# Kernel tuning notes

Measured on AMD Instinct MI355X. Metric: run time of the kernel, lower is better.

The kernel has to match this reference:

```python
import jax, jax.numpy as jnp
import numpy as np

B, S, D, I, C = 4, 512, 512, 1024, 64
BASE_LR = 0.01
EPS = 1e-6


def _rms(x, w):
    return x * jax.lax.rsqrt(jnp.mean(x * x, axis=-1, keepdims=True) + EPS) * w


def _mem_apply(p, x):
    # 2-layer MLP memory: x + RMSNorm(W1 @ silu(W0 @ x))
    h = jax.nn.silu(x @ p["w0"].T)
    y = h @ p["w1"].T
    return x + _rms(y, p["ln"])


def _mem_loss(p, inp, tgt, w):
    # ((target - pred)^2 * theta).mean(-1).sum() over batch; w is scalar theta_t
    pred = _mem_apply(p, inp)
    return jnp.sum(jnp.mean((tgt - pred) ** 2 * w, axis=-1))


def _neural_memory(x, wq, wk, wv, q_norm_w, k_norm_w, alpha_w, alpha_b,
                   theta_w, theta_b, eta_w, eta_b, m_w0, m_w1, m_ln):
    b, s, d = x.shape
    nC = s // C
    params0 = {"w0": m_w0, "w1": m_w1, "ln": m_ln}
    surpr0 = jax.tree_util.tree_map(jnp.zeros_like, params0)
    xs = x.reshape(b, nC, C, d).transpose(1, 0, 2, 3)  # [nC, B, C, D]

    # per-token grads: vmap over sequence dim 1, shared params (in_dims=None)
    grad_fn = jax.vmap(jax.grad(_mem_loss), in_axes=(None, 1, 1, 0))
    idx = jnp.arange(C)

    def step(carry, xc):
        params, surpr = carry
        # adaptive gates: Linear -> sum over batch -> sigmoid (shapes [C])
        al = jax.nn.sigmoid(jnp.sum(xc @ alpha_w.T + alpha_b, axis=0))[:, 0]
        th = jax.nn.sigmoid(jnp.sum(xc @ theta_w.T + theta_b, axis=0))[:, 0] * BASE_LR
        et = jax.nn.sigmoid(jnp.sum(xc @ eta_w.T + eta_b, axis=0))[:, 0]
        k = _rms(jax.nn.silu(xc @ wk.T), k_norm_w)  # [B, C, D]
        v = jax.nn.silu(xc @ wv.T)
        grads = grad_fn(params, k, v, th)  # each leaf [C, *param_shape]
        # eta decay matrix E[m,n] = prod_{i=n+1}^m eta_i for n<=m, else 0
        M0 = jnp.where(idx[:, None] > idx[None, :], et[:, None], 1.0)
        Emat = jnp.where(idx[None, :] <= idx[:, None], jnp.cumprod(M0, axis=0), 0.0)
        c_eta = jnp.cumprod(et)  # prod_{0..m} eta
        beta = 1.0 - al
        bc_last = jnp.cumprod(beta)[-1]
        bt = jnp.cumprod(beta[::-1])[::-1]  # bt[m] = prod_{m..C-1} beta
        w_beta = jnp.concatenate([bt[1:], jnp.ones((1,), et.dtype)])

        def upd(pS, pM, u):
            # S_t = eta_t * S_{t-1} - u_t ; M_t = beta_t * M_{t-1} + S_t (vectorized)
            ex = (slice(None),) + (None,) * pS.ndim
            S_all = c_eta[ex] * pS - jnp.einsum("mn,n...->m...", Emat, u)
            newM = pM * bc_last + jnp.einsum("m,m...->...", w_beta, S_all)
            return newM, S_all[-1]

        res = {n: upd(surpr[n], params[n], grads[n]) for n in params}
        new_params = {n: res[n][0] for n in params}
        new_surpr = {n: res[n][1] for n in params}
        return (new_params, new_surpr), None

    (paramsF, _surprF), _ = jax.lax.scan(step, (params0, surpr0), xs)
    # retrieve from updated memory
    q = _rms(jax.nn.silu(x @ wq.T), q_norm_w)
    return _mem_apply(paramsF, q)


def setup_inputs() -> dict:
    key = jax.random.key(0)
    ks = jax.random.split(key, 12)

    def xavier(k, shape):
        lim = float(np.sqrt(6.0 / (shape[0] + shape[1])))
        return jax.random.uniform(k, shape, jnp.float32, -lim, lim)

    return {
        "x": jax.random.normal(ks[0], (B, S, D), jnp.float32),
        "wq": xavier(ks[1], (D, D)),
        "wk": xavier(ks[2], (D, D)),
        "wv": xavier(ks[3], (D, D)),
        "q_norm_w": jnp.ones((D,), jnp.float32),
        "k_norm_w": jnp.ones((D,), jnp.float32),
        "alpha_w": xavier(ks[4], (1, D)),
        "alpha_b": jnp.zeros((1,), jnp.float32),
        "theta_w": xavier(ks[5], (1, D)),
        "theta_b": jnp.zeros((1,), jnp.float32),
        "eta_w": xavier(ks[6], (1, D)),
        "eta_b": jnp.zeros((1,), jnp.float32),
        "m_w0": xavier(ks[7], (I, D)),
        "m_w1": xavier(ks[8], (D, I)),
        "m_ln": jnp.ones((D,), jnp.float32),
    }


def reference(x, wq, wk, wv, q_norm_w, k_norm_w, alpha_w, alpha_b,
              theta_w, theta_b, eta_w, eta_b, m_w0, m_w1, m_ln):
    return _neural_memory(x, wq, wk, wv, q_norm_w, k_norm_w, alpha_w, alpha_b,
                          theta_w, theta_b, eta_w, eta_b, m_w0, m_w1, m_ln)
```

## Files before the change

### kernel.cpp

```cpp
#include <hip/hip_runtime.h>
#include <math.h>

#define EPS 1e-6f

namespace {

typedef unsigned short u16;
typedef unsigned int u32;
typedef __bf16 bf16x8 __attribute__((ext_vector_type(8)));
typedef float f32x4 __attribute__((ext_vector_type(4)));
typedef u16 u16x8 __attribute__((ext_vector_type(8)));

constexpr int Bb = 4, Ss = 512, Dd = 512, Ii = 1024, Cc = 64;
constexpr int nCk = 8, RowsC = 256, RowsAll = 2048;

__device__ __forceinline__ float sigmoidf_(float x) { return 1.f / (1.f + expf(-x)); }
__device__ __forceinline__ float siluf_(float x)    { return x / (1.f + expf(-x)); }

__device__ __forceinline__ u16 f2bf(float f) {
  u32 u = __float_as_uint(f);
  u32 r = u + 0x7fffu + ((u >> 16) & 1u);
  return (u16)(r >> 16);
}

__device__ __forceinline__ void llds16(const u16* g, u16* l) {
  __builtin_amdgcn_global_load_lds((__attribute__((address_space(1))) void*)g,
                                   (__attribute__((address_space(3))) void*)l,
                                   16, 0, 0);
}

__device__ __forceinline__ void drain_barrier() {
  asm volatile("s_waitcnt vmcnt(0)" ::: "memory");
  __builtin_amdgcn_s_barrier();
}

__device__ __forceinline__ float wave_sum(float v) {
  #pragma unroll
// ... 2 lines not shown
}

__device__ __forceinline__ float block_reduce_sum(float v, float* red) {
  int tid = threadIdx.x;
  red[tid] = v; __syncthreads();
  for (int s = 128; s > 0; s >>= 1) {
    if (tid < s) red[tid] += red[tid + s];
    __syncthreads();
  }
  float r = red[0]; __syncthreads();
  return r;
}

struct WS {
  float *w0c, *Sw0, *w1c, *Sw1, *lnc, *Sln, *tmpK, *Krows, *Vrows,
        *Ybuf, *gyr, *Z0, *alv, *thv, *etv, *wBv, *wEv, *scal, *Qb, *Yr;
  u16 *xcb, *wqb, *wkvb, *w0b, *w1b, *w1tb, *Kb, *KT, *Hb, *Ht,
      *dYb, *dYtW, *dYtE, *dHtW, *dHtE, *Qbb, *Hrb;
};
__host__ __device__ inline WS mkws(char* base) {
  WS s; char* p = base + 256;
#define CF(nm, n) s.nm = (float*)p; p += (size_t)(n) * 4;
#define CU(nm, n) s.nm = (u16*)p;   p += (size_t)(n) * 2;
  CF(w0c, Ii*Dd) CF(Sw0, Ii*Dd) CF(w1c, Dd*Ii) CF(Sw1, Dd*Ii)
  CF(lnc, Dd) CF(Sln, Dd)
  CF(tmpK, (size_t)RowsAll*Dd) CF(Krows, (size_t)RowsAll*Dd) CF(Vrows, (size_t)RowsAll*Dd)
  CF(Ybuf, RowsC*Dd) CF(gyr, RowsC*Dd) CF(Z0, RowsC*Ii)
  CF(alv, Ss) CF(thv, Ss) CF(etv, Ss) CF(wBv, nCk*RowsC) CF(wEv, nCk*RowsC) CF(scal, nCk*4)
  CF(Qb, (size_t)RowsAll*Dd) CF(Yr, (size_t)RowsAll*Dd)
  CU(xcb, (size_t)RowsAll*Dd) CU(wqb, Dd*Dd) CU(wkvb, (size_t)Ii*Dd)
  CU(w0b, (size_t)Ii*Dd) CU(w1b, (size_t)Dd*Ii) CU(w1tb, (size_t)Ii*Dd)
  CU(Kb, (size_t)RowsAll*Dd) CU(KT, (size_t)RowsAll*Dd)
  CU(Hb, RowsC*Ii) CU(Ht, RowsC*Ii)
  CU(dYb, RowsC*Dd) CU(dYtW, RowsC*Dd) CU(dYtE, RowsC*Dd)
  CU(dHtW, RowsC*Ii) CU(dHtE, RowsC*Ii)
  CU(Qbb, (size_t)RowsAll*Dd) CU(Hrb, (size_t)RowsAll*Ii)
#undef CF
#undef CU
  return s;
}

template<int BK, int EPI>
__device__ void tile64(
    u16* smA, u16* smB,
    const u16* __restrict__ A, const u16* __restrict__ Bt,
    int K, int N, int bm, int bn,
    float* C0, float* C1, u16* Cb, u16* CbT, u16* CbT2,
    const float* Z, const float* wB, const float* wE, int trM)
{
  constexpr int CPR = BK / 8;
  constexpr int NISS = (64 * CPR) / 256;
  constexpr int BUF = 64 * BK;
  const int tid = threadIdx.x;
  const int l = tid & 63, lr = l & 15, lq = l >> 4;
  const int w = tid >> 6, wr = w >> 1, wc = w & 1;

  f32x4 acc[2][2];
  #pragma unroll
  for (int i = 0; i < 2; ++i)
    #pragma unroll
    for (int j = 0; j < 2; ++j) acc[i][j] = f32x4{0.f, 0.f, 0.f, 0.f};

  auto stage = [&](int k0, int buf) {
// ... 1 lines not shown
    u16* dB = smB + buf * BUF;
    #pragma unroll
    for (int i = 0; i < NISS; ++i) {
      int e = i * 256 + tid;
      int r = e / CPR, c = (e & (CPR - 1)) ^ (r & (CPR - 1));
      llds16(A  + (size_t)(bm + r) * K + k0 + c * 8, dA + e * 8);
      llds16(Bt + (size_t)(bn + r) * K + k0 + c * 8, dB + e * 8);
    }
  };

  stage(0, 0);
  drain_barrier();
  const int nt = K / BK;
  int cur = 0;
  for (int t = 0; t < nt; ++t) {
    if (t + 1 < nt) stage((t + 1) * BK, cur ^ 1);
    const u16* sA = smA + cur * BUF;
    const u16* sB = smB + cur * BUF;
    #pragma unroll
    for (int kk = 0; kk < BK / 32; ++kk) {
      bf16x8 av[2], bv[2];
      #pragma unroll
      for (int m = 0; m < 2; ++m) {
        int r = wr * 32 + m * 16 + lr;
        int c = (kk * 4 + lq) ^ (r & (CPR - 1));
        av[m] = *reinterpret_cast<const bf16x8*>(&sA[r * BK + c * 8]);
      }
      #pragma unroll
      for (int n = 0; n < 2; ++n) {
        int r = wc * 32 + n * 16 + lr;
        int c = (kk * 4 + lq) ^ (r & (CPR - 1));
        bv[n] = *reinterpret_cast<const bf16x8*>(&sB[r * BK + c * 8]);
      }
      #pragma unroll
      for (int m = 0; m < 2; ++m)
        #pragma unroll
        for (int n = 0; n < 2; ++n)
          acc[m][n] = __builtin_amdgcn_mfma_f32_16x16x32_bf16(av[m], bv[n], acc[m][n], 0, 0, 0);
    }
    drain_barrier();
    cur ^= 1;
  }

  #pragma unroll
  for (int m = 0; m < 2; ++m) {
    int gr0 = bm + wr * 32 + m * 16 + lq * 4;
    float wbq[4], weq[4];
    if (EPI == 3) {
      #pragma unroll
      for (int q = 0; q < 4; ++q) { wbq[q] = wB[gr0 + q]; weq[q] = wE[gr0 + q]; }
    }
    #pragma unroll
    for (int n = 0; n < 2; ++n) {
      int gc = bn + wc * 32 + n * 16 + lr;
      ushort4 t1, t2;
      #pragma unroll
      for (int q = 0; q < 4; ++q) {
        float v = acc[m][n][q];
        size_t idx = (size_t)(gr0 + q) * N + gc;
        if (EPI == 0) {
          C0[idx] = v;
        } else if (EPI == 1) {
          if (gc < Dd) C0[(size_t)(gr0 + q) * Dd + gc] = v;
          else         C1[(size_t)(gr0 + q) * Dd + gc - Dd] = siluf_(v);
        } else if (EPI == 2) {
          C0[idx] = v;
          float h = siluf_(v);
          Cb[idx] = f2bf(h);
          ((u16*)&t1)[q] = f2bf(h);
        } else if (EPI == 3) {
          float z = Z[idx];
          float sg = 1.f / (1.f + expf(-z));
          float dh = v * sg * (1.f + z * (1.f - sg));
          ((u16*)&t1)[q] = f2bf(dh * wbq[q]);
          ((u16*)&t2)[q] = f2bf(dh * weq[q]);
        } else if (EPI == 4) {
          Cb[idx] = f2bf(siluf_(v));
        }
      }
      if (EPI == 2) *reinterpret_cast<ushort4*>(&CbT[(size_t)gc * trM + gr0]) = t1;
      if (EPI == 3) {
        *reinterpret_cast<ushort4*>(&CbT[(size_t)gc * trM + gr0]) = t1;
        *reinterpret_cast<ushort4*>(&CbT2[(size_t)gc * trM + gr0]) = t2;
      }
    }
  }
}

template<int BK, bool TR>
__device__ void gtile64(
    u16* smA, u16* smB, u16* smE,
    const u16* __restrict__ AW, const u16* __restrict__ AE,
    const u16* __restrict__ Bt,
    float* P, float* Sm, u16* Pb, u16* PbT, const float* scal,
    int M, int N, int K, int bm, int bn)
{
  constexpr int CPR = BK / 8;
  constexpr int NISS = (64 * CPR) / 256;
  constexpr int BUF = 64 * BK;
  const int tid = threadIdx.x;
  const int l = tid & 63, lr = l & 15, lq = l >> 4;
  const int w = tid >> 6, wr = w >> 1, wc = w & 1;

  f32x4 aM[2][2], aE[2][2];
// ... 12 lines not shown
    #pragma unroll
    for (int i = 0; i < NISS; ++i) {
      int e = i * 256 + tid;
      int r = e / CPR, c = (e & (CPR - 1)) ^ (r & (CPR - 1));
      llds16(AW + (size_t)(bm + r) * K + k0 + c * 8, dA + e * 8);
      llds16(AE + (size_t)(bm + r) * K + k0 + c * 8, dE + e * 8);
      llds16(Bt + (size_t)(bn + r) * K + k0 + c * 8, dB + e * 8);
    }
  };

  stage(0, 0);
  drain_barrier();
  const int nt = K / BK;
  int cur = 0;
  for (int t = 0; t < nt; ++t) {
    if (t + 1 < nt) stage((t + 1) * BK, cur ^ 1);
    const u16* sA = smA + cur * BUF;
    const u16* sE = smE + cur * BUF;
    const u16* sB = smB + cur * BUF;
    #pragma unroll
    for (int kk = 0; kk < BK / 32; ++kk) {
      bf16x8 awv[2], aev[2], bv[2];
      #pragma unroll
      for (int m = 0; m < 2; ++m) {
        int r = wr * 32 + m * 16 + lr;
        int c = (kk * 4 + lq) ^ (r & (CPR - 1));
        awv[m] = *reinterpret_cast<const bf16x8*>(&sA[r * BK + c * 8]);
        aev[m] = *reinterpret_cast<const bf16x8*>(&sE[r * BK + c * 8]);
      }
      #pragma unroll
      for (int n = 0; n < 2; ++n) {
        int r = wc * 32 + n * 16 + lr;
        int c = (kk * 4 + lq) ^ (r & (CPR - 1));
        bv[n] = *reinterpret_cast<const bf16x8*>(&sB[r * BK + c * 8]);
      }
      #pragma unroll
      for (int m = 0; m < 2; ++m)
        #pragma unroll
        for (int n = 0; n < 2; ++n) {
          aM[m][n] = __builtin_amdgcn_mfma_f32_16x16x32_bf16(awv[m], bv[n], aM[m][n], 0, 0, 0);
          aE[m][n] = __builtin_amdgcn_mfma_f32_16x16x32_bf16(aev[m], bv[n], aE[m][n], 0, 0, 0);
        }
    }
    drain_barrier();
    cur ^= 1;
  }

  float s0 = scal[0], s1 = scal[1], s2 = scal[2];
  #pragma unroll
  for (int m = 0; m < 2; ++m) {
    int gr0 = bm + wr * 32 + m * 16 + lq * 4;
    #pragma unroll
    for (int n = 0; n < 2; ++n) {
      int gc = bn + wc * 32 + n * 16 + lr;
      ushort4 t1;
      #pragma unroll
      for (int q = 0; q < 4; ++q) {
        size_t idx = (size_t)(gr0 + q) * N + gc;
        float p = P[idx], s = Sm[idx];
        float np = s0 * p + s1 * s - aM[m][n][q];
        float ns = s2 * s - aE[m][n][q];
        P[idx] = np; Sm[idx] = ns;
        Pb[idx] = f2bf(np);
        if (TR) ((u16*)&t1)[q] = f2bf(np);
      }
      if (TR) *reinterpret_cast<ushort4*>(&PbT[(size_t)gc * M + gr0]) = t1;
    }
  }
}

template<int BK, int EPI>
__global__ __launch_bounds__(256) void mgemm_k(
    const u16* __restrict__ A, const u16* __restrict__ Bt,
    float* C0, float* C1, u16* Cb, u16* CbT, u16* CbT2,
    const float* Z, const float* wB, const float* wE,
    int M, int N, int K, int trM)
{
  __shared__ __align__(16) u16 sm[4 * 64 * BK];
  tile64<BK, EPI>(sm, sm + 2 * 64 * BK, A, Bt, K, N,
                  blockIdx.y * 64, blockIdx.x * 64,
                  C0, C1, Cb, CbT, CbT2, Z, wB, wE, trM);
}

template<int EPI>
__global__ __launch_bounds__(256) void mgemm128_k(
    const u16* __restrict__ A, const u16* __restrict__ Bt,
    float* C0, u16* Cb, int M, int N, int K)
{
  constexpr int TS = 128, BK = 64;
  constexpr int BUF = TS * BK;
  __shared__ __align__(16) u16 As[2 * BUF];
  __shared__ __align__(16) u16 Bs[2 * BUF];
  const int tid = threadIdx.x;
  const int l = tid & 63, lr = l & 15, lq = l >> 4;
  const int w = tid >> 6, wr = w >> 1, wc = w & 1;
  const int bm = blockIdx.y * TS, bn = blockIdx.x * TS;

  f32x4 acc[4][4];
  #pragma unroll
  for (int i = 0; i < 4; ++i)
    #pragma unroll
    for (int j = 0; j < 4; ++j) acc[i][j] = f32x4{0.f, 0.f, 0.f, 0.f};

  auto stage = [&](int k0, int buf) {
    u16* dA = As + buf * BUF;
    u16* dB = Bs + buf * BUF;
    #pragma unroll
    for (int i = 0; i < 4; ++i) {
      int e = i * 256 + tid;
      int r = e >> 3, c = (e & 7) ^ (r & 7);
      llds16(A  + (size_t)(bm + r) * K + k0 + c * 8, dA + e * 8);
      llds16(Bt + (size_t)(bn + r) * K + k0 + c * 8, dB + e * 8);
    }
  };

  stage(0, 0);
  drain_barrier();
  const int nt = K / BK;
  int cur = 0;
  for (int t = 0; t < nt; ++t) {
    if (t + 1 < nt) stage((t + 1) * BK, cur ^ 1);
    const u16* sA = As + cur * BUF;
    const u16* sB = Bs + cur * BUF;
    #pragma unroll
    for (int kk = 0; kk < 2; ++kk) {
      bf16x8 av[4], bv[4];
      #pragma unroll
      for (int m = 0; m < 4; ++m) {
        int r = wr * 64 + m * 16 + lr;
        int c = (kk * 4 + lq) ^ (r & 7);
        av[m] = *reinterpret_cast<const bf16x8*>(&sA[r * BK + c * 8]);
      }
      #pragma unroll
      for (int n = 0; n < 4; ++n) {
        int r = wc * 64 + n * 16 + lr;
        int c = (kk * 4 + lq) ^ (r & 7);
        bv[n] = *reinterpret_cast<const bf16x8*>(&sB[r * BK + c * 8]);
      }
      #pragma unroll
      for (int m = 0; m < 4; ++m)
        #pragma unroll
        for (int n = 0; n < 4; ++n)
          acc[m][n] = __builtin_amdgcn_mfma_f32_16x16x32_bf16(av[m], bv[n], acc[m][n], 0, 0, 0);
    }
    drain_barrier();
    cur ^= 1;
  }

  #pragma unroll
  for (int m = 0; m < 4; ++m) {
    int gr0 = bm + wr * 64 + m * 16 + lq * 4;
    #pragma unroll
    for (int n = 0; n < 4; ++n) {
      int gc = bn + wc * 64 + n * 16 + lr;
      #pragma unroll
      for (int q = 0; q < 4; ++q) {
        size_t idx = (size_t)(gr0 + q) * N + gc;
        float v = acc[m][n][q];
        if (EPI == 0) C0[idx] = v;
        else          Cb[idx] = f2bf(siluf_(v));
      }
    }
  }
}

template<int BK>
__global__ __launch_bounds__(256) void dh_colsum_k(
    const u16* __restrict__ dYb, const u16* __restrict__ w1tb,
    u16* dHtW, u16* dHtE, const float* Z0,
    const float* wB, const float* wE,
    const float* gyr, float* lnc, float* Sln, const float* scal)
{
  __shared__ __align__(16) u16 sm[4 * 64 * BK];
  int j = blockIdx.x;
  if (j < 64) {
    int tm = j & 3, tn = j >> 2;
    tile64<BK, 3>(sm, sm + 2 * 64 * BK, dYb, w1tb, Dd, Ii, tm * 64, tn * 64,
                  nullptr, nullptr, nullptr, dHtW, dHtE, Z0, wB, wE, RowsC);
  } else {
    int d = (j - 64) * 256 + threadIdx.x;
    float sm2 = 0.f, se2 = 0.f;
    for (int r = 0; r < RowsC; ++r) {
      float vv = gyr[(size_t)r * Dd + d];
      sm2 += wB[r] * vv; se2 += wE[r] * vv;
    }
    float pp = lnc[d], sn = Sln[d];
    lnc[d] = scal[0] * pp + scal[1] * sn - sm2;
    Sln[d] = scal[2] * sn - se2;
  }
}

template<int BK>
__global__ __launch_bounds__(256) void g2_k(
    const u16* __restrict__ dYtW, const u16* __restrict__ dYtE,
    const u16* __restrict__ Ht,
    const u16* __restrict__ dHtW, const u16* __restrict__ dHtE,
    const u16* __restrict__ KTc,
    float* w1c, float* Sw1, u16* w1b, u16* w1tb,
    float* w0c, float* Sw0, u16* w0b,
    const float* scal)
{
  __shared__ __align__(16) u16 sm[6 * 64 * BK];
  int j = blockIdx.x;
  if (j < 128) {
    gtile64<BK, true>(sm, sm + 2 * 64 * BK, sm + 4 * 64 * BK, dYtW, dYtE, Ht,
                      w1c, Sw1, w1b, w1tb, scal, Dd, Ii, RowsC,
                      (j >> 4) * 64, (j & 15) * 64);
  } else {
    j -= 128;
    gtile64<BK, false>(sm, sm + 2 * 64 * BK, sm + 4 * 64 * BK, dHtW, dHtE, KTc,
                       w0c, Sw0, w0b, nullptr, scal, Ii, Dd, RowsC,
                       (j >> 3) * 64, (j & 7) * 64);
  }
}

__global__ __launch_bounds__(256) void init_k(
    const float* __restrict__ wq, const float* __restrict__ wkw,
    const float* __restrict__ wvw, const float* __restrict__ mw0,
    const float* __restrict__ mw1, const float* __restrict__ mln,
    char* ws)
{
  WS S = mkws(ws);
  __shared__ float t[64][65];
  if (blockIdx.x < 128) {
    int j = blockIdx.x;
    int br = (j & 7) * 64, bc = (j >> 3) * 64;
    const int tid = threadIdx.x;
    #pragma unroll
    for (int i = 0; i < 16; ++i) {
      int e = tid + i * 256;
      int r = e >> 6, c = e & 63;
      t[r][c] = mw1[(size_t)(br + r) * Ii + bc + c];
    }
    __syncthreads();
    #pragma unroll
    for (int i = 0; i < 16; ++i) {
      int e = tid + i * 256;
      int rr = e >> 6, cc = e & 63;
      S.w1tb[(size_t)(bc + rr) * Dd + br + cc] = f2bf(t[cc][rr]);
    }
    return;
  }
  const int i0 = (blockIdx.x - 128) * 256 + threadIdx.x;
  const int stride = (gridDim.x - 128) * 256;
  for (int i = i0; i < (Dd * Dd) / 4; i += stride) {
    float4 v = ((const float4*)wq)[i];
    ushort4 o; o.x = f2bf(v.x); o.y = f2bf(v.y); o.z = f2bf(v.z); o.w = f2bf(v.w);
    ((ushort4*)S.wqb)[i] = o;
    v = ((const float4*)wkw)[i];
    o.x = f2bf(v.x); o.y = f2bf(v.y); o.z = f2bf(v.z); o.w = f2bf(v.w);
    ((ushort4*)S.wkvb)[i] = o;
    v = ((const float4*)wvw)[i];
    o.x = f2bf(v.x); o.y = f2bf(v.y); o.z = f2bf(v.z); o.w = f2bf(v.w);
    ((ushort4*)S.wkvb)[i + (Dd * Dd) / 4] = o;
  }
  for (int i = i0; i < (Ii * Dd) / 4; i += stride) {
    float4 z4; z4.x = z4.y = z4.z = z4.w = 0.f;
    float4 v = ((const float4*)mw0)[i];
    ((float4*)S.w0c)[i] = v; ((float4*)S.Sw0)[i] = z4;
    ushort4 o; o.x = f2bf(v.x); o.y = f2bf(v.y); o.z = f2bf(v.z); o.w = f2bf(v.w);
    ((ushort4*)S.w0b)[i] = o;
    v = ((const float4*)mw1)[i];
    ((float4*)S.w1c)[i] = v; ((float4*)S.Sw1)[i] = z4;
    o.x = f2bf(v.x); o.y = f2bf(v.y); o.z = f2bf(v.z); o.w = f2bf(v.w);
    ((ushort4*)S.w1b)[i] = o;
  }
  for (int i = i0; i < Dd; i += stride) { S.lnc[i] = mln[i]; S.Sln[i] = 0.f; }
}

__global__ __launch_bounds__(256) void prep_k(
    const float* __restrict__ x,
    const float* __restrict__ aw, const float* __restrict__ ab,
    const float* __restrict__ tw, const float* __restrict__ tb,
    const float* __restrict__ ew, const float* __restrict__ eb,
    char* ws)
{
  WS S = mkws(ws);
  __shared__ float red[256];
  int s = blockIdx.x, tid = threadIdx.x;
  int ci = s >> 6, t = s & 63;
  float sa = 0.f, st = 0.f, se = 0.f;
  for (int b = 0; b < Bb; ++b) {
    const float* xr = x + ((size_t)b * Ss + s) * Dd;
    u16* dst = S.xcb + ((size_t)(ci * RowsC + b * Cc + t)) * Dd;
    for (int d = tid; d < Dd; d += 256) {
      float v = xr[d];
      dst[d] = f2bf(v);
      sa += v * aw[d]; st += v * tw[d]; se += v * ew[d];
    }
  }
  sa = block_reduce_sum(sa, red);
  st = block_reduce_sum(st, red);
  se = block_reduce_sum(se, red);
  if (tid == 0) {
    S.alv[s] = sigmoidf_(sa + Bb * ab[0]);
    S.thv[s] = sigmoidf_(st + Bb * tb[0]) * 0.01f;
    S.etv[s] = sigmoidf_(se + Bb * eb[0]);
  }
}

__global__ void gate_scan_all_k(char* ws)
{
  if (threadIdx.x != 0) return;
  WS S = mkws(ws);
  int ci = blockIdx.x;
  const float* alc = S.alv + ci * Cc;
  const float* etc_ = S.etv + ci * Cc;
  float beta[Cc], wb[Cc], ce[Cc], E[Cc], T[Cc];
  for (int i = 0; i < Cc; ++i) beta[i] = 1.f - alc[i];
  wb[Cc - 1] = 1.f;
  for (int m = Cc - 2; m >= 0; --m) wb[m] = wb[m + 1] * beta[m + 1];
  float bc_last = wb[0] * beta[0];
  float p = 1.f, A = 0.f;
  for (int m = 0; m < Cc; ++m) { p *= etc_[m]; ce[m] = p; A += wb[m] * ce[m]; }
  E[Cc - 1] = 1.f; T[Cc - 1] = 1.f;
  for (int n = Cc - 2; n >= 0; --n) {
    E[n] = E[n + 1] * etc_[n + 1];
    T[n] = wb[n] + etc_[n + 1] * T[n + 1];
  }
  for (int b = 0; b < Bb; ++b)
    for (int t = 0; t < Cc; ++t) {
      S.wBv[ci * RowsC + b * Cc + t] = T[t];
      S.wEv[ci * RowsC + b * Cc + t] = E[t];
    }
  S.scal[ci * 4 + 0] = bc_last; S.scal[ci * 4 + 1] = A; S.scal[ci * 4 + 2] = ce[Cc - 1];
}

template<bool TR>
__global__ __launch_bounds__(256) void silu_rms4_k(
    const float* __restrict__ in, float* __restrict__ out,
    u16* __restrict__ outb, u16* __restrict__ KT,
    const float* __restrict__ nw)
{
  __shared__ u16 lt[4][Dd];
  const int tid = threadIdx.x, w = tid >> 6, l = tid & 63;
  const int r0 = blockIdx.x * 4;
  const int row = r0 + w, d0 = l * 8;
  const float* ir = in + (size_t)row * Dd + d0;
  float v[8];
  *(float4*)&v[0] = *(const float4*)ir;
  *(float4*)&v[4] = *(const float4*)(ir + 4);
  float ss = 0.f;
  #pragma unroll
  for (int j = 0; j < 8; ++j) { v[j] = siluf_(v[j]); ss += v[j] * v[j]; }
  ss = wave_sum(ss);
  float rr = rsqrtf(ss / (float)Dd + EPS);
  float nv[8];
  *(float4*)&nv[0] = *(const float4*)(nw + d0);
  *(float4*)&nv[4] = *(const float4*)(nw + d0 + 4);
  float y[8]; u16x8 pb;
  #pragma unroll
  for (int j = 0; j < 8; ++j) { y[j] = v[j] * rr * nv[j]; pb[j] = f2bf(y[j]); }
  float* orow = out + (size_t)row * Dd + d0;
  *(float4*)orow       = *(float4*)&y[0];
  *(float4*)(orow + 4) = *(float4*)&y[4];
  *(u16x8*)(outb + (size_t)row * Dd + d0) = pb;
  if (TR) {
    int ci = r0 >> 8, rloc = r0 & 255;
    u16* KTc = KT + (size_t)ci * Dd * RowsC;
    #pragma unroll
    for (int j = 0; j < 8; ++j) lt[w][d0 + j] = pb[j];
    __syncthreads();
    for (int d = tid; d < Dd; d += 256) {
      ushort4 pk;
      pk.x = lt[0][d]; pk.y = lt[1][d]; pk.z = lt[2][d]; pk.w = lt[3][d];
      *reinterpret_cast<ushort4*>(&KTc[(size_t)d * RowsC + rloc]) = pk;
    }
  }
}

__global__ __launch_bounds__(256) void loss_back4_k(
    const float* __restrict__ Kr, const float* __restrict__ Vr,
// ... 100 lines not shown
  const float* qn  = (const float*)d_in[4];
  const float* kn  = (const float*)d_in[5];
  const float* aw  = (const float*)d_in[6];
  const float* ab  = (const float*)d_in[7];
  const float* tw  = (const float*)d_in[8];
  const float* tb  = (const float*)d_in[9];
  const float* ew  = (const float*)d_in[10];
  const float* eb  = (const float*)d_in[11];
  const float* mw0 = (const float*)d_in[12];
  const float* mw1 = (const float*)d_in[13];
  const float* mln = (const float*)d_in[14];
  float* out = (float*)d_out;
  char* ws = (char*)d_ws;
  WS S = mkws(ws);

  init_k<<<1024 + 128, 256, 0, stream>>>(wq, wkw, wvw, mw0, mw1, mln, ws);
  prep_k<<<Ss, 256, 0, stream>>>(x, aw, ab, tw, tb, ew, eb, ws);
  gate_scan_all_k<<<nCk, 64, 0, stream>>>(ws);

  mgemm_k<128, 1><<<dim3(Ii / 64, RowsAll / 64), 256, 0, stream>>>(
      S.xcb, S.wkvb, S.tmpK, S.Vrows, nullptr, nullptr, nullptr,
      nullptr, nullptr, nullptr, RowsAll, Ii, Dd, 0);
  silu_rms4_k<true><<<RowsAll / 4, 256, 0, stream>>>(S.tmpK, S.Krows, S.Kb, S.KT, kn);
  mgemm128_k<0><<<dim3(Dd / 128, RowsAll / 128), 256, 0, stream>>>(
      S.xcb, S.wqb, S.Yr, nullptr, RowsAll, Dd, Dd);
  silu_rms4_k<false><<<RowsAll / 4, 256, 0, stream>>>(S.Yr, S.Qb, S.Qbb, nullptr, qn);

  for (int ci = 0; ci < nCk; ++ci) {
    const u16* Kbc = S.Kb + (size_t)ci * RowsC * Dd;
    const u16* KTc = S.KT + (size_t)ci * Dd * RowsC;
    const float* Krc = S.Krows + (size_t)ci * RowsC * Dd;
    const float* Vrc = S.Vrows + (size_t)ci * RowsC * Dd;
    const float* scc = S.scal + ci * 4;
    const float* wBc = S.wBv + ci * RowsC;
    const float* wEc = S.wEv + ci * RowsC;
    const float* thc = S.thv + ci * Cc;

    mgemm_k<128, 2><<<dim3(Ii / 64, RowsC / 64), 256, 0, stream>>>(
        Kbc, S.w0b, S.Z0, nullptr, S.Hb, S.Ht, nullptr,
        nullptr, nullptr, nullptr, RowsC, Ii, Dd, RowsC);
    mgemm_k<128, 0><<<dim3(Dd / 64, RowsC / 64), 256, 0, stream>>>(
        S.Hb, S.w1b, S.Ybuf, nullptr, nullptr, nullptr, nullptr,
        nullptr, nullptr, nullptr, RowsC, Dd, Ii, 0);
    loss_back4_k<<<RowsC / 4, 256, 0, stream>>>(
        Krc, Vrc, S.Ybuf, S.lnc, thc, wBc, wEc, S.dYb, S.dYtW, S.dYtE, S.gyr);
    dh_colsum_k<128><<<66, 256, 0, stream>>>(
        S.dYb, S.w1tb, S.dHtW, S.dHtE, S.Z0, wBc, wEc, S.gyr, S.lnc, S.Sln, scc);
    g2_k<128><<<256, 256, 0, stream>>>(
        S.dYtW, S.dYtE, S.Ht, S.dHtW, S.dHtE, KTc,
        S.w1c, S.Sw1, S.w1b, S.w1tb, S.w0c, S.Sw0, S.w0b, scc);
  }

  mgemm128_k<4><<<dim3(Ii / 128, RowsAll / 128), 256, 0, stream>>>(
      S.Qbb, S.w0b, nullptr, S.Hrb, RowsAll, Ii, Dd);
  mgemm128_k<0><<<dim3(Dd / 128, RowsAll / 128), 256, 0, stream>>>(
      S.Hrb, S.w1b, S.Yr, nullptr, RowsAll, Dd, Ii);
  final4_k<<<RowsAll / 4, 256, 0, stream>>>(S.Qb, S.Yr, S.lnc, out);
}
```

Before: 429.6 us.

## Fuse setup kernels, merge QKV GEMM, ping-pong w1 and split grad stage

Merges prep, weight-conversion and gate-scan into fewer launches, concatenates Wk/Wv/Wq into one GEMM, and normalises K and Q in a single kernel. In the per-chunk loop, the first GEMM epilogue now stores the bf16 silu derivative instead of the fp32 pre-activation. The w1 copies are double-buffered, so the w1 update can run concurrently with the dH GEMM in one launch, and the w0 update gets its own kernel. BK grows to 256 with single-buffered LDS in the weight-gradient tiles. This cuts launches and memory traffic, but the larger LDS use may lower occupancy and the bf16 derivative loses precision.

```diff
diff --git a/kernel.cpp b/kernel.cpp
--- a/kernel.cpp
+++ b/kernel.cpp
@@ -21,6 +21,9 @@
   u32 u = __float_as_uint(f);
   u32 r = u + 0x7fffu + ((u >> 16) & 1u);
   return (u16)(r >> 16);
+}
+__device__ __forceinline__ float bf2f(u16 u) {
+  return __uint_as_float(((u32)u) << 16);
 }
 
 __device__ __forceinline__ void llds16(const u16* g, u16* l) {
@@ -53,8 +56,8 @@
 
 struct WS {
   float *w0c, *Sw0, *w1c, *Sw1, *lnc, *Sln, *tmpK, *Krows, *Vrows,
-        *Ybuf, *gyr, *Z0, *alv, *thv, *etv, *wBv, *wEv, *scal, *Qb, *Yr;
-  u16 *xcb, *wqb, *wkvb, *w0b, *w1b, *w1tb, *Kb, *KT, *Hb, *Ht,
+        *Ybuf, *gyr, *alv, *thv, *etv, *wBv, *wEv, *scal, *Qb, *Yr;
+  u16 *xcb, *wkvqb, *w0b, *w1b, *w1tb, *Kb, *KT, *Hb, *Ht, *dZb,
       *dYb, *dYtW, *dYtE, *dHtW, *dHtE, *Qbb, *Hrb;
 };
 __host__ __device__ inline WS mkws(char* base) {
@@ -64,13 +67,13 @@
   CF(w0c, Ii*Dd) CF(Sw0, Ii*Dd) CF(w1c, Dd*Ii) CF(Sw1, Dd*Ii)
   CF(lnc, Dd) CF(Sln, Dd)
   CF(tmpK, (size_t)RowsAll*Dd) CF(Krows, (size_t)RowsAll*Dd) CF(Vrows, (size_t)RowsAll*Dd)
-  CF(Ybuf, RowsC*Dd) CF(gyr, RowsC*Dd) CF(Z0, RowsC*Ii)
+  CF(Ybuf, RowsC*Dd) CF(gyr, RowsC*Dd)
   CF(alv, Ss) CF(thv, Ss) CF(etv, Ss) CF(wBv, nCk*RowsC) CF(wEv, nCk*RowsC) CF(scal, nCk*4)
   CF(Qb, (size_t)RowsAll*Dd) CF(Yr, (size_t)RowsAll*Dd)
-  CU(xcb, (size_t)RowsAll*Dd) CU(wqb, Dd*Dd) CU(wkvb, (size_t)Ii*Dd)
-  CU(w0b, (size_t)Ii*Dd) CU(w1b, (size_t)Dd*Ii) CU(w1tb, (size_t)Ii*Dd)
+  CU(xcb, (size_t)RowsAll*Dd) CU(wkvqb, (size_t)3*Dd*Dd)
+  CU(w0b, (size_t)Ii*Dd) CU(w1b, (size_t)2*Dd*Ii) CU(w1tb, (size_t)2*Ii*Dd)
   CU(Kb, (size_t)RowsAll*Dd) CU(KT, (size_t)RowsAll*Dd)
-  CU(Hb, RowsC*Ii) CU(Ht, RowsC*Ii)
+  CU(Hb, RowsC*Ii) CU(Ht, RowsC*Ii) CU(dZb, RowsC*Ii)
   CU(dYb, RowsC*Dd) CU(dYtW, RowsC*Dd) CU(dYtE, RowsC*Dd)
   CU(dHtW, RowsC*Ii) CU(dHtE, RowsC*Ii)
   CU(Qbb, (size_t)RowsAll*Dd) CU(Hrb, (size_t)RowsAll*Ii)
@@ -79,13 +82,14 @@
   return s;
 }
 
-template<int BK, int EPI>
+template<int BK, int NBUF, int EPI>
 __device__ void tile64(
     u16* smA, u16* smB,
     const u16* __restrict__ A, const u16* __restrict__ Bt,
     int K, int N, int bm, int bn,
-    float* C0, float* C1, u16* Cb, u16* CbT, u16* CbT2,
-    const float* Z, const float* wB, const float* wE, int trM)
+    float* C0, float* C1, float* C2,
+    u16* Cb, u16* CbT, u16* CbT2,
+    const u16* Zb, const float* wB, const float* wE, int trM)
 {
   constexpr int CPR = BK / 8;
   constexpr int NISS = (64 * CPR) / 256;
@@ -117,7 +121,7 @@
   const int nt = K / BK;
   int cur = 0;
   for (int t = 0; t < nt; ++t) {
-    if (t + 1 < nt) stage((t + 1) * BK, cur ^ 1);
+    if (t + 1 < nt) stage((t + 1) * BK, (cur ^ 1) & (NBUF - 1));
     const u16* sA = smA + cur * BUF;
     const u16* sB = smB + cur * BUF;
     #pragma unroll
@@ -142,7 +146,7 @@
           acc[m][n] = __builtin_amdgcn_mfma_f32_16x16x32_bf16(av[m], bv[n], acc[m][n], 0, 0, 0);
     }
     drain_barrier();
-    cur ^= 1;
+    cur = (cur ^ 1) & (NBUF - 1);
   }
 
   #pragma unroll
@@ -164,17 +168,19 @@
         if (EPI == 0) {
           C0[idx] = v;
         } else if (EPI == 1) {
-          if (gc < Dd) C0[(size_t)(gr0 + q) * Dd + gc] = v;
-          else         C1[(size_t)(gr0 + q) * Dd + gc - Dd] = siluf_(v);
+          size_t rb = (size_t)(gr0 + q) * Dd;
+          if (gc < Dd)            C0[rb + gc] = v;
+          else if (gc < 2 * Dd)   C1[rb + gc - Dd] = siluf_(v);
+          else                    C2[rb + gc - 2 * Dd] = v;
         } else if (EPI == 2) {
-          C0[idx] = v;
-          float h = siluf_(v);
+          float sg = 1.f / (1.f + expf(-v));
+          float h = v * sg;
+          float ds = sg * (1.f + v * (1.f - sg));
           Cb[idx] = f2bf(h);
+          CbT2[idx] = f2bf(ds);
           ((u16*)&t1)[q] = f2bf(h);
         } else if (EPI == 3) {
-          float z = Z[idx];
-          float sg = 1.f / (1.f + expf(-z));
-          float dh = v * sg * (1.f + z * (1.f - sg));
+          float dh = v * bf2f(Zb[idx]);
           ((u16*)&t1)[q] = f2bf(dh * wbq[q]);
           ((u16*)&t2)[q] = f2bf(dh * weq[q]);
         } else if (EPI == 4) {
@@ -190,7 +196,7 @@
   }
 }
 
-template<int BK, bool TR>
+template<int BK, int NBUF, bool TR>
 __device__ void gtile64(
     u16* smA, u16* smB, u16* smE,
     const u16* __restrict__ AW, const u16* __restrict__ AE,
@@ -233,7 +239,7 @@
   const int nt = K / BK;
   int cur = 0;
   for (int t = 0; t < nt; ++t) {
-    if (t + 1 < nt) stage((t + 1) * BK, cur ^ 1);
+    if (t + 1 < nt) stage((t + 1) * BK, (cur ^ 1) & (NBUF - 1));
     const u16* sA = smA + cur * BUF;
     const u16* sE = smE + cur * BUF;
     const u16* sB = smB + cur * BUF;
@@ -262,7 +268,7 @@
         }
     }
     drain_barrier();
-    cur ^= 1;
+    cur = (cur ^ 1) & (NBUF - 1);
   }
 
   float s0 = scal[0], s1 = scal[1], s2 = scal[2];
@@ -288,115 +294,46 @@
   }
 }
 
-template<int BK, int EPI>
-__global__ __launch_bounds__(256) void mgemm_k(
+
+__global__ __launch_bounds__(256) void z0_k(
     const u16* __restrict__ A, const u16* __restrict__ Bt,
-    float* C0, float* C1, u16* Cb, u16* CbT, u16* CbT2,
-    const float* Z, const float* wB, const float* wE,
-    int M, int N, int K, int trM)
-{
-  __shared__ __align__(16) u16 sm[4 * 64 * BK];
-  tile64<BK, EPI>(sm, sm + 2 * 64 * BK, A, Bt, K, N,
-                  blockIdx.y * 64, blockIdx.x * 64,
-                  C0, C1, Cb, CbT, CbT2, Z, wB, wE, trM);
-}
-
-template<int EPI>
-__global__ __launch_bounds__(256) void mgemm128_k(
-    const u16* __restrict__ A, const u16* __restrict__ Bt,
-    float* C0, u16* Cb, int M, int N, int K)
-{
-  constexpr int TS = 128, BK = 64;
-  constexpr int BUF = TS * BK;
-  __shared__ __align__(16) u16 As[2 * BUF];
-  __shared__ __align__(16) u16 Bs[2 * BUF];
-  const int tid = threadIdx.x;
-  const int l = tid & 63, lr = l & 15, lq = l >> 4;
-  const int w = tid >> 6, wr = w >> 1, wc = w & 1;
-  const int bm = blockIdx.y * TS, bn = blockIdx.x * TS;
-
-  f32x4 acc[4][4];
-  #pragma unroll
-  for (int i = 0; i < 4; ++i)
-    #pragma unroll
-    for (int j = 0; j < 4; ++j) acc[i][j] = f32x4{0.f, 0.f, 0.f, 0.f};
-
-  auto stage = [&](int k0, int buf) {
-    u16* dA = As + buf * BUF;
-    u16* dB = Bs + buf * BUF;
-    #pragma unroll
-    for (int i = 0; i < 4; ++i) {
-      int e = i * 256 + tid;
-      int r = e >> 3, c = (e & 7) ^ (r & 7);
-      llds16(A  + (size_t)(bm + r) * K + k0 + c * 8, dA + e * 8);
-      llds16(Bt + (size_t)(bn + r) * K + k0 + c * 8, dB + e * 8);
-    }
-  };
-
-  stage(0, 0);
-  drain_barrier();
-  const int nt = K / BK;
-  int cur = 0;
-  for (int t = 0; t < nt; ++t) {
-    if (t + 1 < nt) stage((t + 1) * BK, cur ^ 1);
-    const u16* sA = As + cur * BUF;
-    const u16* sB = Bs + cur * BUF;
-    #pragma unroll
-    for (int kk = 0; kk < 2; ++kk) {
-      bf16x8 av[4], bv[4];
-      #pragma unroll
-      for (int m = 0; m < 4; ++m) {
-        int r = wr * 64 + m * 16 + lr;
-        int c = (kk * 4 + lq) ^ (r & 7);
-        av[m] = *reinterpret_cast<const bf16x8*>(&sA[r * BK + c * 8]);
-      }
-      #pragma unroll
-      for (int n = 0; n < 4; ++n) {
-        int r = wc * 64 + n * 16 + lr;
-        int c = (kk * 4 + lq) ^ (r & 7);
-        bv[n] = *reinterpret_cast<const bf16x8*>(&sB[r * BK + c * 8]);
-      }
-      #pragma unroll
-      for (int m = 0; m < 4; ++m)
-        #pragma unroll
-        for (int n = 0; n < 4; ++n)
-          acc[m][n] = __builtin_amdgcn_mfma_f32_16x16x32_bf16(av[m], bv[n], acc[m][n], 0, 0, 0);
-    }
-    drain_barrier();
-    cur ^= 1;
-  }
-
-  #pragma unroll
-  for (int m = 0; m < 4; ++m) {
-    int gr0 = bm + wr * 64 + m * 16 + lq * 4;
-    #pragma unroll
-    for (int n = 0; n < 4; ++n) {
-      int gc = bn + wc * 64 + n * 16 + lr;
-      #pragma unroll
-      for (int q = 0; q < 4; ++q) {
-        size_t idx = (size_t)(gr0 + q) * N + gc;
-        float v = acc[m][n][q];
-        if (EPI == 0) C0[idx] = v;
-        else          Cb[idx] = f2bf(siluf_(v));
-      }
-    }
-  }
-}
-
-template<int BK>
-__global__ __launch_bounds__(256) void dh_colsum_k(
-    const u16* __restrict__ dYb, const u16* __restrict__ w1tb,
-    u16* dHtW, u16* dHtE, const float* Z0,
-    const float* wB, const float* wE,
-    const float* gyr, float* lnc, float* Sln, const float* scal)
-{
-  __shared__ __align__(16) u16 sm[4 * 64 * BK];
+    u16* Hb, u16* Ht, u16* dZb)
+{
+  __shared__ __align__(16) u16 sm[4 * 64 * 256];
+  tile64<256, 2, 2>(sm, sm + 2 * 64 * 256, A, Bt, Dd, Ii,
+                    blockIdx.y * 64, blockIdx.x * 64,
+                    nullptr, nullptr, nullptr, Hb, Ht, dZb,
+                    nullptr, nullptr, nullptr, RowsC);
+}
+
+__global__ __launch_bounds__(256) void y_k(
+    const u16* __restrict__ A, const u16* __restrict__ Bt, float* C0)
+{
+  __shared__ __align__(16) u16 sm[4 * 64 * 256];
+  tile64<256, 2, 0>(sm, sm + 2 * 64 * 256, A, Bt, Ii, Dd,
+                    blockIdx.y * 64, blockIdx.x * 64,
+                    C0, nullptr, nullptr, nullptr, nullptr, nullptr,
+                    nullptr, nullptr, nullptr, 0);
+}
+
+__global__ __launch_bounds__(256) void s4_k(
+    const u16* __restrict__ dYb, const u16* __restrict__ w1t_cur,
+    const u16* __restrict__ dZb, u16* dHtW, u16* dHtE,
+    const float* __restrict__ gyr, float* lnc, float* Sln,
+    const u16* __restrict__ dYtW, const u16* __restrict__ dYtE,
+    const u16* __restrict__ Ht,
+    float* w1c, float* Sw1, u16* w1b_new, u16* w1t_new,
+    const float* wB, const float* wE, const float* scal)
+{
+  __shared__ __align__(16) u16 sm[4 * 64 * 256];
   int j = blockIdx.x;
   if (j < 64) {
     int tm = j & 3, tn = j >> 2;
-    tile64<BK, 3>(sm, sm + 2 * 64 * BK, dYb, w1tb, Dd, Ii, tm * 64, tn * 64,
-                  nullptr, nullptr, nullptr, dHtW, dHtE, Z0, wB, wE, RowsC);
-  } else {
+    tile64<256, 2, 3>(sm, sm + 2 * 64 * 256, dYb, w1t_cur, Dd, Ii,
+                      tm * 64, tn * 64,
+                      nullptr, nullptr, nullptr, nullptr, dHtW, dHtE,
+                      dZb, wB, wE, RowsC);
+  } else if (j < 66) {
     int d = (j - 64) * 256 + threadIdx.x;
     float sm2 = 0.f, se2 = 0.f;
     for (int r = 0; r < RowsC; ++r) {
@@ -406,123 +343,43 @@
     float pp = lnc[d], sn = Sln[d];
     lnc[d] = scal[0] * pp + scal[1] * sn - sm2;
     Sln[d] = scal[2] * sn - se2;
-  }
-}
-
-template<int BK>
-__global__ __launch_bounds__(256) void g2_k(
-    const u16* __restrict__ dYtW, const u16* __restrict__ dYtE,
-    const u16* __restrict__ Ht,
+  } else {
+    int q = j - 66;
+    gtile64<256, 1, true>(sm, sm + 64 * 256, sm + 2 * 64 * 256,
+                          dYtW, dYtE, Ht, w1c, Sw1, w1b_new, w1t_new,
+                          scal, Dd, Ii, RowsC, (q >> 4) * 64, (q & 15) * 64);
+  }
+}
+
+__global__ __launch_bounds__(256) void g2b_k(
     const u16* __restrict__ dHtW, const u16* __restrict__ dHtE,
     const u16* __restrict__ KTc,
-    float* w1c, float* Sw1, u16* w1b, u16* w1tb,
-    float* w0c, float* Sw0, u16* w0b,
-    const float* scal)
-{
-  __shared__ __align__(16) u16 sm[6 * 64 * BK];
+    float* w0c, float* Sw0, u16* w0b, const float* scal)
+{
+  __shared__ __align__(16) u16 sm[3 * 64 * 256];
   int j = blockIdx.x;
-  if (j < 128) {
-    gtile64<BK, true>(sm, sm + 2 * 64 * BK, sm + 4 * 64 * BK, dYtW, dYtE, Ht,
-                      w1c, Sw1, w1b, w1tb, scal, Dd, Ii, RowsC,
-                      (j >> 4) * 64, (j & 15) * 64);
-  } else {
-    j -= 128;
-    gtile64<BK, false>(sm, sm + 2 * 64 * BK, sm + 4 * 64 * BK, dHtW, dHtE, KTc,
-                       w0c, Sw0, w0b, nullptr, scal, Ii, Dd, RowsC,
-                       (j >> 3) * 64, (j & 7) * 64);
-  }
-}
-
-__global__ __launch_bounds__(256) void init_k(
-    const float* __restrict__ wq, const float* __restrict__ wkw,
-    const float* __restrict__ wvw, const float* __restrict__ mw0,
-    const float* __restrict__ mw1, const float* __restrict__ mln,
-    char* ws)
-{
-  WS S = mkws(ws);
-  __shared__ float t[64][65];
-  if (blockIdx.x < 128) {
-    int j = blockIdx.x;
-    int br = (j & 7) * 64, bc = (j >> 3) * 64;
-    const int tid = threadIdx.x;
-    #pragma unroll
-    for (int i = 0; i < 16; ++i) {
-      int e = tid + i * 256;
-      int r = e >> 6, c = e & 63;
-      t[r][c] = mw1[(size_t)(br + r) * Ii + bc + c];
-    }
-    __syncthreads();
-    #pragma unroll
-    for (int i = 0; i < 16; ++i) {
-      int e = tid + i * 256;
-      int rr = e >> 6, cc = e & 63;
-      S.w1tb[(size_t)(bc + rr) * Dd + br + cc] = f2bf(t[cc][rr]);
-    }
+  gtile64<256, 1, false>(sm, sm + 64 * 256, sm + 2 * 64 * 256,
+                         dHtW, dHtE, KTc, w0c, Sw0, w0b, nullptr,
+                         scal, Ii, Dd, RowsC, (j >> 3) * 64, (j & 7) * 64);
+}
+
+__global__ __launch_bounds__(256) void kvq_k(
+    const u16* __restrict__ xcb, const u16* __restrict__ wkvqb,
+    float* tmpK, float* Vrows, float* Yq, char* ws)
+{
+  __shared__ __align__(16) u16 sm[4 * 64 * 128];
+  int j = blockIdx.x;
+  if (j < 768) {
+    int tn = j % 24, tm = j / 24;
+    tile64<128, 2, 1>(sm, sm + 2 * 64 * 128, xcb, wkvqb, Dd, 3 * Dd,
+                      tm * 64, tn * 64,
+                      tmpK, Vrows, Yq, nullptr, nullptr, nullptr,
+                      nullptr, nullptr, nullptr, 0);
     return;
   }
-  const int i0 = (blockIdx.x - 128) * 256 + threadIdx.x;
-  const int stride = (gridDim.x - 128) * 256;
-  for (int i = i0; i < (Dd * Dd) / 4; i += stride) {
-    float4 v = ((const float4*)wq)[i];
-    ushort4 o; o.x = f2bf(v.x); o.y = f2bf(v.y); o.z = f2bf(v.z); o.w = f2bf(v.w);
-    ((ushort4*)S.wqb)[i] = o;
-    v = ((const float4*)wkw)[i];
-    o.x = f2bf(v.x); o.y = f2bf(v.y); o.z = f2bf(v.z); o.w = f2bf(v.w);
-    ((ushort4*)S.wkvb)[i] = o;
-    v = ((const float4*)wvw)[i];
-    o.x = f2bf(v.x); o.y = f2bf(v.y); o.z = f2bf(v.z); o.w = f2bf(v.w);
-    ((ushort4*)S.wkvb)[i + (Dd * Dd) / 4] = o;
-  }
-  for (int i = i0; i < (Ii * Dd) / 4; i += stride) {
-    float4 z4; z4.x = z4.y = z4.z = z4.w = 0.f;
-    float4 v = ((const float4*)mw0)[i];
-    ((float4*)S.w0c)[i] = v; ((float4*)S.Sw0)[i] = z4;
-    ushort4 o; o.x = f2bf(v.x); o.y = f2bf(v.y); o.z = f2bf(v.z); o.w = f2bf(v.w);
-    ((ushort4*)S.w0b)[i] = o;
-    v = ((const float4*)mw1)[i];
-    ((float4*)S.w1c)[i] = v; ((float4*)S.Sw1)[i] = z4;
-    o.x = f2bf(v.x); o.y = f2bf(v.y); o.z = f2bf(v.z); o.w = f2bf(v.w);
-    ((ushort4*)S.w1b)[i] = o;
-  }
-  for (int i = i0; i < Dd; i += stride) { S.lnc[i] = mln[i]; S.Sln[i] = 0.f; }
-}
-
-__global__ __launch_bounds__(256) void prep_k(
-    const float* __restrict__ x,
-    const float* __restrict__ aw, const float* __restrict__ ab,
-    const float* __restrict__ tw, const float* __restrict__ tb,
-    const float* __restrict__ ew, const float* __restrict__ eb,
-    char* ws)
-{
-  WS S = mkws(ws);
-  __shared__ float red[256];
-  int s = blockIdx.x, tid = threadIdx.x;
-  int ci = s >> 6, t = s & 63;
-  float sa = 0.f, st = 0.f, se = 0.f;
-  for (int b = 0; b < Bb; ++b) {
-    const float* xr = x + ((size_t)b * Ss + s) * Dd;
-    u16* dst = S.xcb + ((size_t)(ci * RowsC + b * Cc + t)) * Dd;
-    for (int d = tid; d < Dd; d += 256) {
-      float v = xr[d];
-      dst[d] = f2bf(v);
-      sa += v * aw[d]; st += v * tw[d]; se += v * ew[d];
-    }
-  }
-  sa = block_reduce_sum(sa, red);
-  st = block_reduce_sum(st, red);
-  se = block_reduce_sum(se, red);
-  if (tid == 0) {
-    S.alv[s] = sigmoidf_(sa + Bb * ab[0]);
-    S.thv[s] = sigmoidf_(st + Bb * tb[0]) * 0.01f;
-    S.etv[s] = sigmoidf_(se + Bb * eb[0]);
-  }
-}
-
-__global__ void gate_scan_all_k(char* ws)
-{
   if (threadIdx.x != 0) return;
   WS S = mkws(ws);
-  int ci = blockIdx.x;
+  int ci = j - 768;
   const float* alc = S.alv + ci * Cc;
   const float* etc_ = S.etv + ci * Cc;
   float beta[Cc], wb[Cc], ce[Cc], E[Cc], T[Cc];
@@ -545,36 +402,203 @@
   S.scal[ci * 4 + 0] = bc_last; S.scal[ci * 4 + 1] = A; S.scal[ci * 4 + 2] = ce[Cc - 1];
 }
 
-template<bool TR>
-__global__ __launch_bounds__(256) void silu_rms4_k(
-    const float* __restrict__ in, float* __restrict__ out,
-    u16* __restrict__ outb, u16* __restrict__ KT,
-    const float* __restrict__ nw)
+template<int EPI>
+__global__ __launch_bounds__(256) void mgemm128_k(
+    const u16* __restrict__ A, const u16* __restrict__ Bt,
+    float* C0, u16* Cb, int M, int N, int K)
+{
+  constexpr int TS = 128, BK = 64;
+  constexpr int BUF = TS * BK;
+  __shared__ __align__(16) u16 As[2 * BUF];
+  __shared__ __align__(16) u16 Bs[2 * BUF];
+  const int tid = threadIdx.x;
+  const int l = tid & 63, lr = l & 15, lq = l >> 4;
+  const int w = tid >> 6, wr = w >> 1, wc = w & 1;
+  const int bm = blockIdx.y * TS, bn = blockIdx.x * TS;
+
+  f32x4 acc[4][4];
+  #pragma unroll
+  for (int i = 0; i < 4; ++i)
+    #pragma unroll
+    for (int j = 0; j < 4; ++j) acc[i][j] = f32x4{0.f, 0.f, 0.f, 0.f};
+
+  auto stage = [&](int k0, int buf) {
+    u16* dA = As + buf * BUF;
+    u16* dB = Bs + buf * BUF;
+    #pragma unroll
+    for (int i = 0; i < 4; ++i) {
+      int e = i * 256 + tid;
+      int r = e >> 3, c = (e & 7) ^ (r & 7);
+      llds16(A  + (size_t)(bm + r) * K + k0 + c * 8, dA + e * 8);
+      llds16(Bt + (size_t)(bn + r) * K + k0 + c * 8, dB + e * 8);
+    }
+  };
+
+  stage(0, 0);
+  drain_barrier();
+  const int nt = K / BK;
+  int cur = 0;
+  for (int t = 0; t < nt; ++t) {
+    if (t + 1 < nt) stage((t + 1) * BK, cur ^ 1);
+    const u16* sA = As + cur * BUF;
+    const u16* sB = Bs + cur * BUF;
+    #pragma unroll
+    for (int kk = 0; kk < 2; ++kk) {
+      bf16x8 av[4], bv[4];
+      #pragma unroll
+      for (int m = 0; m < 4; ++m) {
+        int r = wr * 64 + m * 16 + lr;
+        int c = (kk * 4 + lq) ^ (r & 7);
+        av[m] = *reinterpret_cast<const bf16x8*>(&sA[r * BK + c * 8]);
+      }
+      #pragma unroll
+      for (int n = 0; n < 4; ++n) {
+        int r = wc * 64 + n * 16 + lr;
+        int c = (kk * 4 + lq) ^ (r & 7);
+        bv[n] = *reinterpret_cast<const bf16x8*>(&sB[r * BK + c * 8]);
+      }
+      #pragma unroll
+      for (int m = 0; m < 4; ++m)
+        #pragma unroll
+        for (int n = 0; n < 4; ++n)
+          acc[m][n] = __builtin_amdgcn_mfma_f32_16x16x32_bf16(av[m], bv[n], acc[m][n], 0, 0, 0);
+    }
+    drain_barrier();
+    cur ^= 1;
+  }
+
+  #pragma unroll
+  for (int m = 0; m < 4; ++m) {
+    int gr0 = bm + wr * 64 + m * 16 + lq * 4;
+    #pragma unroll
+    for (int n = 0; n < 4; ++n) {
+      int gc = bn + wc * 64 + n * 16 + lr;
+      #pragma unroll
+      for (int q = 0; q < 4; ++q) {
+        size_t idx = (size_t)(gr0 + q) * N + gc;
+        float v = acc[m][n][q];
+        if (EPI == 0) C0[idx] = v;
+        else          Cb[idx] = f2bf(siluf_(v));
+      }
+    }
+  }
+}
+
+__global__ __launch_bounds__(256) void init_k(
+    const float* __restrict__ x,
+    const float* __restrict__ aw, const float* __restrict__ ab,
+    const float* __restrict__ tw, const float* __restrict__ tb,
+    const float* __restrict__ ew, const float* __restrict__ eb,
+    const float* __restrict__ wq, const float* __restrict__ wkw,
+    const float* __restrict__ wvw, const float* __restrict__ mw0,
+    const float* __restrict__ mw1, const float* __restrict__ mln,
+    char* ws)
+{
+  WS S = mkws(ws);
+  const int tid = threadIdx.x;
+  if (blockIdx.x < 512) {
+    __shared__ float red[256];
+    int s = blockIdx.x;
+    int ci = s >> 6, t = s & 63;
+    float sa = 0.f, st = 0.f, se = 0.f;
+    for (int b = 0; b < Bb; ++b) {
+      const float* xr = x + ((size_t)b * Ss + s) * Dd;
+      u16* dst = S.xcb + ((size_t)(ci * RowsC + b * Cc + t)) * Dd;
+      for (int d = tid; d < Dd; d += 256) {
+        float v = xr[d];
+        dst[d] = f2bf(v);
+        sa += v * aw[d]; st += v * tw[d]; se += v * ew[d];
+      }
+    }
+    sa = block_reduce_sum(sa, red);
+    st = block_reduce_sum(st, red);
+    se = block_reduce_sum(se, red);
+    if (tid == 0) {
+      S.alv[s] = sigmoidf_(sa + Bb * ab[0]);
+      S.thv[s] = sigmoidf_(st + Bb * tb[0]) * 0.01f;
+      S.etv[s] = sigmoidf_(se + Bb * eb[0]);
+    }
+    return;
+  }
+  if (blockIdx.x < 640) {
+    __shared__ float t[64][65];
+    int tt = blockIdx.x - 512;
+    int br = (tt & 7) * 64, bc = (tt >> 3) * 64;
+    #pragma unroll
+    for (int i = 0; i < 16; ++i) {
+      int e = tid + i * 256;
+      int r = e >> 6, c = e & 63;
+      t[r][c] = mw1[(size_t)(br + r) * Ii + bc + c];
+    }
+    __syncthreads();
+    #pragma unroll
+    for (int i = 0; i < 16; ++i) {
+      int e = tid + i * 256;
+      int rr = e >> 6, cc = e & 63;
+      S.w1tb[(size_t)(bc + rr) * Dd + br + cc] = f2bf(t[cc][rr]);
+    }
+    return;
+  }
+  const int i0 = (blockIdx.x - 640) * 256 + tid;
+  const int stride = 512 * 256;
+  for (int i = i0; i < (Dd * Dd) / 4; i += stride) {
+    float4 v = ((const float4*)wkw)[i];
+    ushort4 o; o.x = f2bf(v.x); o.y = f2bf(v.y); o.z = f2bf(v.z); o.w = f2bf(v.w);
+    ((ushort4*)S.wkvqb)[i] = o;
+    v = ((const float4*)wvw)[i];
+    o.x = f2bf(v.x); o.y = f2bf(v.y); o.z = f2bf(v.z); o.w = f2bf(v.w);
+    ((ushort4*)S.wkvqb)[i + (Dd * Dd) / 4] = o;
+    v = ((const float4*)wq)[i];
+    o.x = f2bf(v.x); o.y = f2bf(v.y); o.z = f2bf(v.z); o.w = f2bf(v.w);
+    ((ushort4*)S.wkvqb)[i + (Dd * Dd) / 2] = o;
+  }
+  for (int i = i0; i < (Ii * Dd) / 4; i += stride) {
+    float4 z4; z4.x = z4.y = z4.z = z4.w = 0.f;
+    float4 v = ((const float4*)mw0)[i];
+    ((float4*)S.w0c)[i] = v; ((float4*)S.Sw0)[i] = z4;
+    ushort4 o; o.x = f2bf(v.x); o.y = f2bf(v.y); o.z = f2bf(v.z); o.w = f2bf(v.w);
+    ((ushort4*)S.w0b)[i] = o;
+    v = ((const float4*)mw1)[i];
+    ((float4*)S.w1c)[i] = v; ((float4*)S.Sw1)[i] = z4;
+    o.x = f2bf(v.x); o.y = f2bf(v.y); o.z = f2bf(v.z); o.w = f2bf(v.w);
+    ((ushort4*)S.w1b)[i] = o;
+  }
+  for (int i = i0; i < Dd; i += stride) { S.lnc[i] = mln[i]; S.Sln[i] = 0.f; }
+}
+
+__global__ __launch_bounds__(256) void norm2_k(
+    const float* __restrict__ tmpK, const float* __restrict__ Yq,
+    float* Krows, u16* Kb, u16* KT,
+    float* Qb, u16* Qbb,
+    const float* __restrict__ kn, const float* __restrict__ qn)
 {
   __shared__ u16 lt[4][Dd];
   const int tid = threadIdx.x, w = tid >> 6, l = tid & 63;
-  const int r0 = blockIdx.x * 4;
+  const bool isQ = blockIdx.x >= 512;
+  const int r0 = (isQ ? (int)blockIdx.x - 512 : (int)blockIdx.x) * 4;
   const int row = r0 + w, d0 = l * 8;
-  const float* ir = in + (size_t)row * Dd + d0;
+  const float* in = (isQ ? Yq : tmpK) + (size_t)row * Dd + d0;
+  const float* nw = (isQ ? qn : kn) + d0;
   float v[8];
-  *(float4*)&v[0] = *(const float4*)ir;
-  *(float4*)&v[4] = *(const float4*)(ir + 4);
+  *(float4*)&v[0] = *(const float4*)in;
+  *(float4*)&v[4] = *(const float4*)(in + 4);
   float ss = 0.f;
   #pragma unroll
   for (int j = 0; j < 8; ++j) { v[j] = siluf_(v[j]); ss += v[j] * v[j]; }
   ss = wave_sum(ss);
   float rr = rsqrtf(ss / (float)Dd + EPS);
   float nv[8];
-  *(float4*)&nv[0] = *(const float4*)(nw + d0);
-  *(float4*)&nv[4] = *(const float4*)(nw + d0 + 4);
+  *(float4*)&nv[0] = *(const float4*)nw;
+  *(float4*)&nv[4] = *(const float4*)(nw + 4);
   float y[8]; u16x8 pb;
   #pragma unroll
   for (int j = 0; j < 8; ++j) { y[j] = v[j] * rr * nv[j]; pb[j] = f2bf(y[j]); }
-  float* orow = out + (size_t)row * Dd + d0;
-  *(float4*)orow       = *(float4*)&y[0];
-  *(float4*)(orow + 4) = *(float4*)&y[4];
-  *(u16x8*)(outb + (size_t)row * Dd + d0) = pb;
-  if (TR) {
+  float* outf = (isQ ? Qb : Krows) + (size_t)row * Dd + d0;
+  u16* outb = (isQ ? Qbb : Kb) + (size_t)row * Dd + d0;
+  *(float4*)outf       = *(float4*)&y[0];
+  *(float4*)(outf + 4) = *(float4*)&y[4];
+  *(u16x8*)outb = pb;
+  if (!isQ) {
     int ci = r0 >> 8, rloc = r0 & 255;
     u16* KTc = KT + (size_t)ci * Dd * RowsC;
     #pragma unroll
@@ -705,19 +729,14 @@
   char* ws = (char*)d_ws;
   WS S = mkws(ws);
 
-  init_k<<<1024 + 128, 256, 0, stream>>>(wq, wkw, wvw, mw0, mw1, mln, ws);
-  prep_k<<<Ss, 256, 0, stream>>>(x, aw, ab, tw, tb, ew, eb, ws);
-  gate_scan_all_k<<<nCk, 64, 0, stream>>>(ws);
-
-  mgemm_k<128, 1><<<dim3(Ii / 64, RowsAll / 64), 256, 0, stream>>>(
-      S.xcb, S.wkvb, S.tmpK, S.Vrows, nullptr, nullptr, nullptr,
-      nullptr, nullptr, nullptr, RowsAll, Ii, Dd, 0);
-  silu_rms4_k<true><<<RowsAll / 4, 256, 0, stream>>>(S.tmpK, S.Krows, S.Kb, S.KT, kn);
-  mgemm128_k<0><<<dim3(Dd / 128, RowsAll / 128), 256, 0, stream>>>(
-      S.xcb, S.wqb, S.Yr, nullptr, RowsAll, Dd, Dd);
-  silu_rms4_k<false><<<RowsAll / 4, 256, 0, stream>>>(S.Yr, S.Qb, S.Qbb, nullptr, qn);
+  init_k<<<1152, 256, 0, stream>>>(x, aw, ab, tw, tb, ew, eb,
+                                   wq, wkw, wvw, mw0, mw1, mln, ws);
+  kvq_k<<<776, 256, 0, stream>>>(S.xcb, S.wkvqb, S.tmpK, S.Vrows, S.Yr, ws);
+  norm2_k<<<1024, 256, 0, stream>>>(S.tmpK, S.Yr, S.Krows, S.Kb, S.KT,
+                                    S.Qb, S.Qbb, kn, qn);
 
   for (int ci = 0; ci < nCk; ++ci) {
+    const int p = ci & 1;
     const u16* Kbc = S.Kb + (size_t)ci * RowsC * Dd;
     const u16* KTc = S.KT + (size_t)ci * Dd * RowsC;
     const float* Krc = S.Krows + (size_t)ci * RowsC * Dd;
@@ -726,20 +745,23 @@
     const float* wBc = S.wBv + ci * RowsC;
     const float* wEc = S.wEv + ci * RowsC;
     const float* thc = S.thv + ci * Cc;
-
-    mgemm_k<128, 2><<<dim3(Ii / 64, RowsC / 64), 256, 0, stream>>>(
-        Kbc, S.w0b, S.Z0, nullptr, S.Hb, S.Ht, nullptr,
-        nullptr, nullptr, nullptr, RowsC, Ii, Dd, RowsC);
-    mgemm_k<128, 0><<<dim3(Dd / 64, RowsC / 64), 256, 0, stream>>>(
-        S.Hb, S.w1b, S.Ybuf, nullptr, nullptr, nullptr, nullptr,
-        nullptr, nullptr, nullptr, RowsC, Dd, Ii, 0);
+    u16* w1b_cur = S.w1b + (size_t)p * Dd * Ii;
+    u16* w1b_new = S.w1b + (size_t)(p ^ 1) * Dd * Ii;
+    u16* w1t_cur = S.w1tb + (size_t)p * Ii * Dd;
+    u16* w1t_new = S.w1tb + (size_t)(p ^ 1) * Ii * Dd;
+
+    z0_k<<<dim3(Ii / 64, RowsC / 64), 256, 0, stream>>>(
+        Kbc, S.w0b, S.Hb, S.Ht, S.dZb);
+    y_k<<<dim3(Dd / 64, RowsC / 64), 256, 0, stream>>>(
+        S.Hb, w1b_cur, S.Ybuf);
     loss_back4_k<<<RowsC / 4, 256, 0, stream>>>(
         Krc, Vrc, S.Ybuf, S.lnc, thc, wBc, wEc, S.dYb, S.dYtW, S.dYtE, S.gyr);
-    dh_colsum_k<128><<<66, 256, 0, stream>>>(
-        S.dYb, S.w1tb, S.dHtW, S.dHtE, S.Z0, wBc, wEc, S.gyr, S.lnc, S.Sln, scc);
-    g2_k<128><<<256, 256, 0, stream>>>(
-        S.dYtW, S.dYtE, S.Ht, S.dHtW, S.dHtE, KTc,
-        S.w1c, S.Sw1, S.w1b, S.w1tb, S.w0c, S.Sw0, S.w0b, scc);
+    s4_k<<<194, 256, 0, stream>>>(
+        S.dYb, w1t_cur, S.dZb, S.dHtW, S.dHtE, S.gyr, S.lnc, S.Sln,
+        S.dYtW, S.dYtE, S.Ht, S.w1c, S.Sw1, w1b_new, w1t_new,
+        wBc, wEc, scc);
+    g2b_k<<<128, 256, 0, stream>>>(
+        S.dHtW, S.dHtE, KTc, S.w0c, S.Sw0, S.w0b, scc);
   }
 
   mgemm128_k<4><<<dim3(Ii / 128, RowsAll / 128), 256, 0, stream>>>(
```

New measurement: 393.7 us. 8.4% less time.
